# Performance work log

Hardware: AMD Instinct MI355X
Metric: run time of the kernel (lower is better)

## Reference

```python
import jax, jax.numpy as jnp
import numpy as np

GAMMA = 4  # channel groups (s)


def setup_inputs() -> dict:
    key = jax.random.key(0)
    k1, k2, k3, k4 = jax.random.split(key, 4)
    b, w, n, c = 16, 128, 256, 128  # batch, windows, win_size, channels
    x = jax.random.normal(k1, (b, w, n, c), dtype=jnp.float32)
    att_std = 0.01
    attention_centers = att_std * jax.random.normal(k2, (GAMMA, 1), dtype=jnp.float32)
    attention_spreads = 1.0 + att_std * jax.random.normal(k3, (GAMMA, 1), dtype=jnp.float32)
    token_proj_n_bias = 0.01 * jax.random.normal(k4, (1, n, 1), dtype=jnp.float32)
    return {"x": x, "attention_centers": attention_centers,
            "attention_spreads": attention_spreads,
            "token_proj_n_bias": token_proj_n_bias}


def _rel_indices(n):
    idx = jnp.arange(n, dtype=jnp.float32)
    d = idx[None, :] - idx[:, None]          # (n, n)
    return jnp.stack([d, d * d], axis=-1)     # (n, n, 2): [indx, indx^2]


def reference(x, attention_centers, attention_spreads, token_proj_n_bias):
    b, w, n, c = x.shape
    s = attention_centers.shape[0]
    v = c // s
    # pos_proj = -1/2 * [-2*delta*inv_cov, inv_cov]  -> (s, 2)
    pos_proj = -0.5 * jnp.concatenate(
        [-2.0 * attention_centers * attention_spreads, attention_spreads], axis=-1)
    rel = _rel_indices(n)                                   # (n, n, 2)
    pos_score = jnp.einsum('mnd,sd->mns', rel, pos_proj)    # (m, n, s)
    posmap = jax.nn.softmax(pos_score, axis=1)              # softmax over n
    xr = x.reshape(b, w, n, v, s)
    out = jnp.einsum('mns,bwnvs->bwmvs', posmap, xr)        # contract tokens n
    out = out + token_proj_n_bias[None, :, :, :, None]       # (1,1,n,1,1) broadcast
    return out.reshape(b, w, n, c)
```

## Files before the change

kernel.cpp:

```cpp
#include <hip/hip_runtime.h>
#include <hip/hip_bf16.h>


#define N_TOK 256
#define C_CH  128
#define NV    32
#define HW    5
#define TAPS  11
#define PMPAD 16
#define MCHUNK 64
#define ROWS  (MCHUNK + 2*HW)
#define XFL4  (ROWS * NV)

typedef const __attribute__((address_space(1))) void gvoid_t;
typedef __attribute__((address_space(3))) void       lvoid_t;

__global__ void pm_build_kernel(const float* __restrict__ centers,
                                const float* __restrict__ spreads,
                                float* __restrict__ pmb) {
    const int m    = blockIdx.x;
    const int lane = threadIdx.x;
    const int n    = m + lane - HW;
    const bool valid = (lane < TAPS) && ((unsigned)n < N_TOK);
    const float dd = (float)(lane - HW);

    float e[4];
#pragma unroll
    for (int s = 0; s < 4; ++s) {
        const float ctr = centers[s];
        const float spr = spreads[s];
        const float sc = (ctr * spr) * dd - 0.5f * spr * dd * dd;
        e[s] = valid ? expf(sc) : 0.0f;
    }
#pragma unroll
    for (int s = 0; s < 4; ++s) {
        float v = e[s];
#pragma unroll
        for (int off = 32; off; off >>= 1) v += __shfl_xor(v, off, 64);
        e[s] = e[s] / __shfl(v, 0, 64);
    }
    if (lane < PMPAD) {
        reinterpret_cast<float4*>(pmb)[m * PMPAD + lane] =
            make_float4(e[0], e[1], e[2], e[3]);
    }
}

__global__ __launch_bounds__(256, 2)
void pm_apply_kernel(const float* __restrict__ x,
                     const float* __restrict__ pmb,
                     const float* __restrict__ bias,
                     float* __restrict__ out) {
    const int m0   = blockIdx.x * MCHUNK;
    const int bw   = blockIdx.y;
    const int row0 = m0 - HW;
    const int tid  = threadIdx.x;

    __shared__ float4 lds_x[XFL4];
    __shared__ float4 lds_pmi[PMPAD];
    __shared__ float4 lds_pme[8 * PMPAD];

    const float* xb = x + (size_t)bw * (N_TOK * C_CH);
    const float4* __restrict__ pm4 = reinterpret_cast<const float4*>(pmb);

#pragma unroll
    for (int i = 0; i < 9; ++i) {
        const int idx = tid + i * 256;
        const int r = idx >> 5;
        const int v = idx & 31;
        int n = row0 + r;
        n = n < 0 ? 0 : (n > N_TOK - 1 ? N_TOK - 1 : n);
        __builtin_amdgcn_global_load_lds((gvoid_t*)(xb + n * C_CH + v * 4),
                                         (lvoid_t*)&lds_x[idx], 16, 0, 0);
    }
    if (tid < 64) {
        const int idx = 2304 + tid;
        const int r = idx >> 5;
        const int v = idx & 31;
        int n = row0 + r;
        n = n > N_TOK - 1 ? N_TOK - 1 : n;
        __builtin_amdgcn_global_load_lds((gvoid_t*)(xb + n * C_CH + v * 4),
                                         (lvoid_t*)&lds_x[idx], 16, 0, 0);
    }

    if (tid < PMPAD) lds_pmi[tid] = pm4[128 * PMPAD + tid];
    const bool edgeblk = (m0 == 0) || (m0 == 192);
    if (edgeblk && tid >= 128 && tid < 256) {
        const int t = tid - 128;
        const int ebase = (m0 == 0) ? 0 : 248;
        lds_pme[t] = pm4[ebase * PMPAD + t];
    }

    __syncthreads();

    const int vg    = tid & 15;
    const int mslot = tid >> 4;
    const int mloc  = mslot * 4;
    const int mbase = m0 + mloc;

    float4 w[TAPS];
#pragma unroll
    for (int t = 0; t < TAPS; ++t) w[t] = lds_pmi[t];

    float4 acc[4][2];
#pragma unroll
    for (int mi = 0; mi < 4; ++mi) {
        const float bv = bias[mbase + mi];
        acc[mi][0] = make_float4(bv, bv, bv, bv);
        acc[mi][1] = acc[mi][0];
    }

    const bool edge = (m0 == 0 && mslot < 2) || (m0 == 192 && mslot >= 14);
    if (!edge) {
#pragma unroll
        for (int nr = 0; nr < 14; ++nr) {
            const int rbase = (mloc + nr) * NV;
            const float4 x0 = lds_x[rbase + vg];
            const float4 x1 = lds_x[rbase + vg + 16];
#pragma unroll
            for (int mi = 0; mi < 4; ++mi) {
                const int d = nr - mi;
                if (d >= 0 && d < TAPS) {
                    acc[mi][0].x += w[d].x * x0.x;
                    acc[mi][0].y += w[d].y * x0.y;
                    acc[mi][0].z += w[d].z * x0.z;
                    acc[mi][0].w += w[d].w * x0.w;
                    acc[mi][1].x += w[d].x * x1.x;
                    acc[mi][1].y += w[d].y * x1.y;
                    acc[mi][1].z += w[d].z * x1.z;
                    acc[mi][1].w += w[d].w * x1.w;
                }
            }
        }
    } else {
        const int ebase = (m0 == 0) ? 0 : 248;
#pragma unroll
        for (int mi = 0; mi < 4; ++mi) {
            const float4* pmrow = lds_pme + (mbase - ebase + mi) * PMPAD;
#pragma unroll
            for (int t = 0; t < TAPS; ++t) {
                const float4 wt = pmrow[t];
                const int rbase = (mloc + mi + t) * NV;
                const float4 x0 = lds_x[rbase + vg];
                const float4 x1 = lds_x[rbase + vg + 16];
                acc[mi][0].x += wt.x * x0.x;
                acc[mi][0].y += wt.y * x0.y;
                acc[mi][0].z += wt.z * x0.z;
                acc[mi][0].w += wt.w * x0.w;
                acc[mi][1].x += wt.x * x1.x;
                acc[mi][1].y += wt.y * x1.y;
                acc[mi][1].z += wt.z * x1.z;
                acc[mi][1].w += wt.w * x1.w;
            }
        }
    }

    float4* ob = reinterpret_cast<float4*>(out + (size_t)bw * (N_TOK * C_CH));
#pragma unroll
    for (int mi = 0; mi < 4; ++mi) {
        ob[(mbase + mi) * NV + vg] = acc[mi][0];
        ob[(mbase + mi) * NV + vg + 16] = acc[mi][1];
    }
}

extern "C" void kernel_launch(void* const* d_in, const int* in_sizes, int n_in,
                              void* d_out, int out_size, void* d_ws, size_t ws_size,
                              hipStream_t stream) {
    const float* x       = (const float*)d_in[0];
    const float* centers = (const float*)d_in[1];
    const float* spreads = (const float*)d_in[2];
    const float* bias    = (const float*)d_in[3];
    float* out = (float*)d_out;
    float* pmb = (float*)d_ws;

    pm_build_kernel<<<dim3(N_TOK), dim3(64), 0, stream>>>(centers, spreads, pmb);

    const int n_bw = 16 * 128;
    pm_apply_kernel<<<dim3(N_TOK / MCHUNK, n_bw), dim3(256), 0, stream>>>(
        x, pmb, bias, out);
}
```

Measured before the change: 107.8 us.

## Process a whole window per block with double-buffered LDS tile prefetch

The apply kernel now gives each block one full (batch, window) slice of 256 tokens instead of one 64-token chunk. It walks the four chunks in sequence and issues the async global-to-LDS load for the next chunk before computing the current one, using two LDS buffers. Edge position-map rows for both ends are staged once per block. This aims to hide global load latency behind the FMA work and cut per-block setup and halo overhead. In exchange there are four times fewer blocks, LDS use per block doubles, and the in-loop bias loads may force vmcnt waits that serialise against the prefetch and undo the overlap.

New measurement: 136.8 us. +26.8%, slower.

```diff
diff --git a/kernel.cpp b/kernel.cpp
--- a/kernel.cpp
+++ b/kernel.cpp
@@ -45,23 +45,9 @@
     }
 }
 
-__global__ __launch_bounds__(256, 2)
-void pm_apply_kernel(const float* __restrict__ x,
-                     const float* __restrict__ pmb,
-                     const float* __restrict__ bias,
-                     float* __restrict__ out) {
-    const int m0   = blockIdx.x * MCHUNK;
-    const int bw   = blockIdx.y;
-    const int row0 = m0 - HW;
-    const int tid  = threadIdx.x;
-
-    __shared__ float4 lds_x[XFL4];
-    __shared__ float4 lds_pmi[PMPAD];
-    __shared__ float4 lds_pme[8 * PMPAD];
-
-    const float* xb = x + (size_t)bw * (N_TOK * C_CH);
-    const float4* __restrict__ pm4 = reinterpret_cast<const float4*>(pmb);
-
+static __device__ __forceinline__ void stage_tile(const float* __restrict__ xb,
+                                                  int tid, int row0,
+                                                  float4* dst) {
 #pragma unroll
     for (int i = 0; i < 9; ++i) {
         const int idx = tid + i * 256;
@@ -70,7 +56,7 @@
         int n = row0 + r;
         n = n < 0 ? 0 : (n > N_TOK - 1 ? N_TOK - 1 : n);
         __builtin_amdgcn_global_load_lds((gvoid_t*)(xb + n * C_CH + v * 4),
-                                         (lvoid_t*)&lds_x[idx], 16, 0, 0);
+                                         (lvoid_t*)&dst[idx], 16, 0, 0);
     }
     if (tid < 64) {
         const int idx = 2304 + tid;
@@ -79,86 +65,113 @@
         int n = row0 + r;
         n = n > N_TOK - 1 ? N_TOK - 1 : n;
         __builtin_amdgcn_global_load_lds((gvoid_t*)(xb + n * C_CH + v * 4),
-                                         (lvoid_t*)&lds_x[idx], 16, 0, 0);
+                                         (lvoid_t*)&dst[idx], 16, 0, 0);
     }
+}
 
+__global__ __launch_bounds__(256, 2)
+void pm_apply_kernel(const float* __restrict__ x,
+                     const float* __restrict__ pmb,
+                     const float* __restrict__ bias,
+                     float* __restrict__ out) {
+    const int bw  = blockIdx.x;
+    const int tid = threadIdx.x;
+
+    __shared__ float4 lds_x[2 * XFL4];
+    __shared__ float4 lds_pmi[PMPAD];
+    __shared__ float4 lds_pme[2 * 8 * PMPAD];
+
+    const float* xb = x + (size_t)bw * (N_TOK * C_CH);
+    const float4* __restrict__ pm4 = reinterpret_cast<const float4*>(pmb);
+
+    stage_tile(xb, tid, -HW, lds_x);
     if (tid < PMPAD) lds_pmi[tid] = pm4[128 * PMPAD + tid];
-    const bool edgeblk = (m0 == 0) || (m0 == 192);
-    if (edgeblk && tid >= 128 && tid < 256) {
-        const int t = tid - 128;
-        const int ebase = (m0 == 0) ? 0 : 248;
-        lds_pme[t] = pm4[ebase * PMPAD + t];
+    {
+        const int mm = (tid < 128) ? (tid >> 4) : (248 + ((tid - 128) >> 4));
+        lds_pme[tid] = pm4[mm * PMPAD + (tid & 15)];
     }
-
     __syncthreads();
 
     const int vg    = tid & 15;
     const int mslot = tid >> 4;
     const int mloc  = mslot * 4;
-    const int mbase = m0 + mloc;
 
     float4 w[TAPS];
 #pragma unroll
     for (int t = 0; t < TAPS; ++t) w[t] = lds_pmi[t];
 
-    float4 acc[4][2];
+    float4* ob = reinterpret_cast<float4*>(out + (size_t)bw * (N_TOK * C_CH));
+
 #pragma unroll
-    for (int mi = 0; mi < 4; ++mi) {
-        const float bv = bias[mbase + mi];
-        acc[mi][0] = make_float4(bv, bv, bv, bv);
-        acc[mi][1] = acc[mi][0];
-    }
+    for (int ch = 0; ch < 4; ++ch) {
+        const float4* xt = lds_x + (ch & 1) * XFL4;
 
-    const bool edge = (m0 == 0 && mslot < 2) || (m0 == 192 && mslot >= 14);
-    if (!edge) {
+        if (ch < 3)
+            stage_tile(xb, tid, (ch + 1) * MCHUNK - HW,
+                       lds_x + ((ch + 1) & 1) * XFL4);
+
+        const int mbase = ch * MCHUNK + mloc;
+
+        float4 acc[4][2];
 #pragma unroll
-        for (int nr = 0; nr < 14; ++nr) {
-            const int rbase = (mloc + nr) * NV;
-            const float4 x0 = lds_x[rbase + vg];
-            const float4 x1 = lds_x[rbase + vg + 16];
+        for (int mi = 0; mi < 4; ++mi) {
+            const float bv = bias[mbase + mi];
+            acc[mi][0] = make_float4(bv, bv, bv, bv);
+            acc[mi][1] = acc[mi][0];
+        }
+
+        const bool edge = (ch == 0 && mslot < 2) || (ch == 3 && mslot >= 14);
+        if (!edge) {
+#pragma unroll
+            for (int nr = 0; nr < 14; ++nr) {
+                const int rbase = (mloc + nr) * NV;
+                const float4 x0 = xt[rbase + vg];
+                const float4 x1 = xt[rbase + vg + 16];
+#pragma unroll
+                for (int mi = 0; mi < 4; ++mi) {
+                    const int d = nr - mi;
+                    if (d >= 0 && d < TAPS) {
+                        acc[mi][0].x += w[d].x * x0.x;
+                        acc[mi][0].y += w[d].y * x0.y;
+                        acc[mi][0].z += w[d].z * x0.z;
+                        acc[mi][0].w += w[d].w * x0.w;
+                        acc[mi][1].x += w[d].x * x1.x;
+                        acc[mi][1].y += w[d].y * x1.y;
+                        acc[mi][1].z += w[d].z * x1.z;
+                        acc[mi][1].w += w[d].w * x1.w;
+                    }
+                }
+            }
+        } else {
+            const int eoff = (ch == 0) ? (mbase) : (mbase - 248 + 8);
 #pragma unroll
             for (int mi = 0; mi < 4; ++mi) {
-                const int d = nr - mi;
-                if (d >= 0 && d < TAPS) {
-                    acc[mi][0].x += w[d].x * x0.x;
-                    acc[mi][0].y += w[d].y * x0.y;
-                    acc[mi][0].z += w[d].z * x0.z;
-                    acc[mi][0].w += w[d].w * x0.w;
-                    acc[mi][1].x += w[d].x * x1.x;
-                    acc[mi][1].y += w[d].y * x1.y;
-                    acc[mi][1].z += w[d].z * x1.z;
-                    acc[mi][1].w += w[d].w * x1.w;
+                const float4* pmrow = lds_pme + (eoff + mi) * PMPAD;
+#pragma unroll
+                for (int t = 0; t < TAPS; ++t) {
+                    const float4 wt = pmrow[t];
+                    const int rbase = (mloc + mi + t) * NV;
+                    const float4 x0 = xt[rbase + vg];
+                    const float4 x1 = xt[rbase + vg + 16];
+                    acc[mi][0].x += wt.x * x0.x;
+                    acc[mi][0].y += wt.y * x0.y;
+                    acc[mi][0].z += wt.z * x0.z;
+                    acc[mi][0].w += wt.w * x0.w;
+                    acc[mi][1].x += wt.x * x1.x;
+                    acc[mi][1].y += wt.y * x1.y;
+                    acc[mi][1].z += wt.z * x1.z;
+                    acc[mi][1].w += wt.w * x1.w;
                 }
             }
         }
-    } else {
-        const int ebase = (m0 == 0) ? 0 : 248;
+
 #pragma unroll
         for (int mi = 0; mi < 4; ++mi) {
-            const float4* pmrow = lds_pme + (mbase - ebase + mi) * PMPAD;
-#pragma unroll
-            for (int t = 0; t < TAPS; ++t) {
-                const float4 wt = pmrow[t];
-                const int rbase = (mloc + mi + t) * NV;
-                const float4 x0 = lds_x[rbase + vg];
-                const float4 x1 = lds_x[rbase + vg + 16];
-                acc[mi][0].x += wt.x * x0.x;
-                acc[mi][0].y += wt.y * x0.y;
-                acc[mi][0].z += wt.z * x0.z;
-                acc[mi][0].w += wt.w * x0.w;
-                acc[mi][1].x += wt.x * x1.x;
-                acc[mi][1].y += wt.y * x1.y;
-                acc[mi][1].z += wt.z * x1.z;
-                acc[mi][1].w += wt.w * x1.w;
-            }
+            ob[(mbase + mi) * NV + vg]      = acc[mi][0];
+            ob[(mbase + mi) * NV + vg + 16] = acc[mi][1];
         }
-    }
 
-    float4* ob = reinterpret_cast<float4*>(out + (size_t)bw * (N_TOK * C_CH));
-#pragma unroll
-    for (int mi = 0; mi < 4; ++mi) {
-        ob[(mbase + mi) * NV + vg] = acc[mi][0];
-        ob[(mbase + mi) * NV + vg + 16] = acc[mi][1];
+        __syncthreads();
     }
 }
 
@@ -175,6 +188,5 @@
     pm_build_kernel<<<dim3(N_TOK), dim3(64), 0, stream>>>(centers, spreads, pmb);
 
     const int n_bw = 16 * 128;
-    pm_apply_kernel<<<dim3(N_TOK / MCHUNK, n_bw), dim3(256), 0, stream>>>(
-        x, pmb, bias, out);
+    pm_apply_kernel<<<dim3(n_bw), dim3(256), 0, stream>>>(x, pmb, bias, out);
 }
```

## Switch apply kernel to single-wavefront blocks over 16-row tiles without barriers

Applied to the files above, without the earlier changes.

Each apply block shrinks from 256 threads covering 64 output rows to a single 64-lane wavefront covering 16 rows, launched on a flattened 1D grid. Because a block is now one wave, __syncthreads is replaced by an explicit vmcnt wait. The interior weights are loaded through the direct global-to-LDS path, and edge rows read their weights straight from global memory. The aim is to remove barrier stalls and raise occupancy and scheduling flexibility. The cost is a larger halo fraction, since 26 rows are loaded per 16 outputs instead of 74 per 64, which adds redundant global reads.

Result: slower. 139.1 us (+29.0%).

```diff
diff --git a/kernel.cpp b/kernel.cpp
--- a/kernel.cpp
+++ b/kernel.cpp
@@ -8,9 +8,9 @@
 #define HW    5
 #define TAPS  11
 #define PMPAD 16
-#define MCHUNK 64
-#define ROWS  (MCHUNK + 2*HW)
-#define XFL4  (ROWS * NV)
+#define WM    16
+#define WROWS (WM + 2*HW)
+#define WFL4  (WROWS * NV)
 
 typedef const __attribute__((address_space(1))) void gvoid_t;
 typedef __attribute__((address_space(3))) void       lvoid_t;
@@ -45,26 +45,26 @@
     }
 }
 
-__global__ __launch_bounds__(256, 2)
+__global__ __launch_bounds__(64)
 void pm_apply_kernel(const float* __restrict__ x,
                      const float* __restrict__ pmb,
                      const float* __restrict__ bias,
                      float* __restrict__ out) {
-    const int m0   = blockIdx.x * MCHUNK;
-    const int bw   = blockIdx.y;
+    const int tile = blockIdx.x & 15;
+    const int bw   = blockIdx.x >> 4;
+    const int lane = threadIdx.x;
+    const int m0   = tile * WM;
     const int row0 = m0 - HW;
-    const int tid  = threadIdx.x;
 
-    __shared__ float4 lds_x[XFL4];
-    __shared__ float4 lds_pmi[PMPAD];
-    __shared__ float4 lds_pme[8 * PMPAD];
+    __shared__ float4 lds_x[WFL4];
+    __shared__ float4 lds_pmi[64];
 
     const float* xb = x + (size_t)bw * (N_TOK * C_CH);
     const float4* __restrict__ pm4 = reinterpret_cast<const float4*>(pmb);
 
 #pragma unroll
-    for (int i = 0; i < 9; ++i) {
-        const int idx = tid + i * 256;
+    for (int i = 0; i < 13; ++i) {
+        const int idx = lane + i * 64;
         const int r = idx >> 5;
         const int v = idx & 31;
         int n = row0 + r;
@@ -72,29 +72,16 @@
         __builtin_amdgcn_global_load_lds((gvoid_t*)(xb + n * C_CH + v * 4),
                                          (lvoid_t*)&lds_x[idx], 16, 0, 0);
     }
-    if (tid < 64) {
-        const int idx = 2304 + tid;
-        const int r = idx >> 5;
-        const int v = idx & 31;
-        int n = row0 + r;
-        n = n > N_TOK - 1 ? N_TOK - 1 : n;
-        __builtin_amdgcn_global_load_lds((gvoid_t*)(xb + n * C_CH + v * 4),
-                                         (lvoid_t*)&lds_x[idx], 16, 0, 0);
-    }
+    __builtin_amdgcn_global_load_lds(
+        (gvoid_t*)(pmb + 128 * (PMPAD * 4) + (lane & 15) * 4),
+        (lvoid_t*)&lds_pmi[lane], 16, 0, 0);
 
-    if (tid < PMPAD) lds_pmi[tid] = pm4[128 * PMPAD + tid];
-    const bool edgeblk = (m0 == 0) || (m0 == 192);
-    if (edgeblk && tid >= 128 && tid < 256) {
-        const int t = tid - 128;
-        const int ebase = (m0 == 0) ? 0 : 248;
-        lds_pme[t] = pm4[ebase * PMPAD + t];
-    }
+    asm volatile("s_waitcnt vmcnt(0)" ::: "memory");
+    __builtin_amdgcn_sched_barrier(0);
 
-    __syncthreads();
-
-    const int vg    = tid & 15;
-    const int mslot = tid >> 4;
-    const int mloc  = mslot * 4;
+    const int vg    = lane & 15;
+    const int ms    = lane >> 4;
+    const int mloc  = ms * 4;
     const int mbase = m0 + mloc;
 
     float4 w[TAPS];
@@ -109,7 +96,7 @@
         acc[mi][1] = acc[mi][0];
     }
 
-    const bool edge = (m0 == 0 && mslot < 2) || (m0 == 192 && mslot >= 14);
+    const bool edge = (tile == 0 && ms < 2) || (tile == 15 && ms >= 2);
     if (!edge) {
 #pragma unroll
         for (int nr = 0; nr < 14; ++nr) {
@@ -132,10 +119,9 @@
             }
         }
     } else {
-        const int ebase = (m0 == 0) ? 0 : 248;
 #pragma unroll
         for (int mi = 0; mi < 4; ++mi) {
-            const float4* pmrow = lds_pme + (mbase - ebase + mi) * PMPAD;
+            const float4* pmrow = pm4 + (mbase + mi) * PMPAD;
 #pragma unroll
             for (int t = 0; t < TAPS; ++t) {
                 const float4 wt = pmrow[t];
@@ -157,7 +143,7 @@
     float4* ob = reinterpret_cast<float4*>(out + (size_t)bw * (N_TOK * C_CH));
 #pragma unroll
     for (int mi = 0; mi < 4; ++mi) {
-        ob[(mbase + mi) * NV + vg] = acc[mi][0];
+        ob[(mbase + mi) * NV + vg]      = acc[mi][0];
         ob[(mbase + mi) * NV + vg + 16] = acc[mi][1];
     }
 }
@@ -174,7 +160,6 @@
 
     pm_build_kernel<<<dim3(N_TOK), dim3(64), 0, stream>>>(centers, spreads, pmb);
 
-    const int n_bw = 16 * 128;
-    pm_apply_kernel<<<dim3(N_TOK / MCHUNK, n_bw), dim3(256), 0, stream>>>(
-        x, pmb, bias, out);
+    const int n_blocks = (16 * 128) * 16;
+    pm_apply_kernel<<<dim3(n_blocks), dim3(64), 0, stream>>>(x, pmb, bias, out);
 }
```
